# Kernel optimization log

Measured on AMD Instinct MI355X. Metric: run time of the kernel, lower is better.

The kernel has to match this reference:

```python
import jax, jax.numpy as jnp
import numpy as np

DIM = 256
N_QUERY = 4096
N_KEY = 128
SIGMA_PRIOR = 1.0
TEMP = 1.0
LN_EPS = 1e-5


def setup_inputs() -> dict:
    key = jax.random.key(0)
    ks = jax.random.split(key, 16)
    s = 1.0 / np.sqrt(2 * DIM)
    sp = 1.0 / np.sqrt(DIM)
    return {
        "Q": jax.random.normal(ks[0], (N_QUERY, DIM), jnp.float32),
        "K": jax.random.normal(ks[1], (N_QUERY, N_KEY, DIM), jnp.float32),
        "V": jax.random.normal(ks[2], (N_QUERY, N_KEY, DIM), jnp.float32),
        "eps": jax.random.normal(ks[3], (N_QUERY, N_KEY), jnp.float32),
        # mu_posterior_layer: Linear(2*dim,1) split into Q-half and K-half
        "w_mu_q": jax.random.normal(ks[4], (DIM,), jnp.float32) * s,
        "w_mu_k": jax.random.normal(ks[5], (DIM,), jnp.float32) * s,
        "b_mu": jax.random.normal(ks[6], (), jnp.float32) * s,
        # logvar_posterior_layer: Linear(2*dim,1) split
        "w_lv_q": jax.random.normal(ks[7], (DIM,), jnp.float32) * s,
        "w_lv_k": jax.random.normal(ks[8], (DIM,), jnp.float32) * s,
        "b_lv": jax.random.normal(ks[9], (), jnp.float32) * s,
        # mu_prior_layer: Linear(dim,dim) -> ReLU -> Linear(dim,1)
        "W_pr1": jax.random.normal(ks[10], (DIM, DIM), jnp.float32) * sp,
        "b_pr1": jax.random.normal(ks[11], (DIM,), jnp.float32) * sp,
        "w_pr2": jax.random.normal(ks[12], (DIM,), jnp.float32) * sp,
        "b_pr2": jax.random.normal(ks[13], (), jnp.float32) * sp,
        # LayerNorm(dim)
        "gamma": jnp.ones((DIM,), jnp.float32),
        "beta": jnp.zeros((DIM,), jnp.float32),
    }


def reference(Q, K, V, eps, w_mu_q, w_mu_k, b_mu, w_lv_q, w_lv_k, b_lv,
              W_pr1, b_pr1, w_pr2, b_pr2, gamma, beta):
    # ---- prior: small MLP over K -> (n_query, n_key) ----
    h = jax.nn.relu(jnp.einsum('qkd,ed->qke', K, W_pr1) + b_pr1)
    mu_prior = jnp.einsum('qke,e->qk', h, w_pr2) + b_pr2
    mu_prior = mu_prior - SIGMA_PRIOR ** 2 / 2
    sigma_prior = SIGMA_PRIOR
    # ---- posterior: Linear(2*dim,1) on cat([Q_expanded, K]) == split matmuls ----
    q_mu = Q @ w_mu_q                           # (n_query,)
    q_lv = Q @ w_lv_q
    logvar_post = q_lv[:, None] + jnp.einsum('qkd,d->qk', K, w_lv_k) + b_lv
    sigma_post = jnp.exp(0.5 * logvar_post)
    mu_post = q_mu[:, None] + jnp.einsum('qkd,d->qk', K, w_mu_k) + b_mu
    mu_post = mu_post - sigma_post ** 2 / 2
    # ---- KL divergence (mean over all scores) ----
    kl = jnp.mean(jnp.log(sigma_prior / sigma_post)
                  + (sigma_post ** 2 + (mu_post - mu_prior) ** 2) / (2 * sigma_prior ** 2)
                  - 0.5)
    # ---- reparameterized sample (note: original divides by temp twice) ----
    samples = jnp.exp(mu_post + sigma_post * eps) / TEMP
    samples = samples / TEMP
    weights = jax.nn.softmax(samples, axis=-1)   # (n_query, n_key)
    # ---- weighted sum over keys + LayerNorm ----
    context = jnp.einsum('qk,qkd->qd', weights, V)
    mean = jnp.mean(context, axis=-1, keepdims=True)
    var = jnp.mean((context - mean) ** 2, axis=-1, keepdims=True)
    context = (context - mean) * jax.lax.rsqrt(var + LN_EPS) * gamma + beta
    return (context, kl)
```

## Files before the change

kernel.cpp:

```cpp
#include <hip/hip_runtime.h>
#include <hip/hip_bf16.h>
#include <stdint.h>

#define NQ 4096
#define NK 128
#define DIM 256

typedef __attribute__((ext_vector_type(4))) float f32x4;
typedef __attribute__((ext_vector_type(8))) __bf16 bf16x8;
typedef __attribute__((ext_vector_type(8))) unsigned short ushort8;

__device__ __forceinline__ unsigned short f2bf(float x) {
    union { float f; unsigned u; } v; v.f = x;
    unsigned r = v.u + 0x7FFFu + ((v.u >> 16) & 1u);
    return (unsigned short)(r >> 16);
}

__global__ void prep_pack(const float* __restrict__ Wpr1, ushort* __restrict__ Bp) {
    int t = blockIdx.x * 256 + threadIdx.x;
    int lane = t & 63;
    int fid = t >> 6;
    int ctl = fid >> 3;
    int kt  = fid & 7;
    int e = ctl * 16 + (lane & 15);
    int d = kt * 32 + (lane >> 4) * 8;
    const float* src = Wpr1 + (size_t)e * DIM + d;
    ushort* dst = Bp + ((size_t)fid * 64 + lane) * 8;
#pragma unroll
    for (int j = 0; j < 8; j++) dst[j] = f2bf(src[j]);
}

__global__ void prep_qdots(const float* __restrict__ Q,
                           const float* __restrict__ wmq,
                           const float* __restrict__ wlq,
                           float* __restrict__ qmu, float* __restrict__ qlv) {
    int q = blockIdx.x * 4 + (threadIdx.x >> 6);
    int lane = threadIdx.x & 63;
    const float* Qr = Q + (size_t)q * DIM;
    float dm = 0.f, dl = 0.f;
#pragma unroll
    for (int i = lane; i < DIM; i += 64) {
        float x = Qr[i];
        dm += x * wmq[i];
        dl += x * wlq[i];
    }
#pragma unroll
    for (int s = 32; s; s >>= 1) { dm += __shfl_xor(dm, s); dl += __shfl_xor(dl, s); }
    if (lane == 0) { qmu[q] = dm; qlv[q] = dl; }
}

__global__ __launch_bounds__(512, 4) void fused_main(
    const float* __restrict__ K, const float* __restrict__ V,
    const float* __restrict__ eps,
    const float* __restrict__ wmk, const float* __restrict__ bmu_p,
    const float* __restrict__ wlk, const float* __restrict__ blv_p,
    const float* __restrict__ bp1, const float* __restrict__ wp2,
    const float* __restrict__ bp2_p,
    const float* __restrict__ gamma, const float* __restrict__ beta,
    const ushort* __restrict__ Bp,
    const float* __restrict__ qmu, const float* __restrict__ qlv,
    float* __restrict__ klpart, float* __restrict__ out) {

    __shared__ __align__(16) char bigbuf[32768];
    __shared__ __align__(16) float wmk_s[DIM], wlk_s[DIM];
    __shared__ __align__(16) float bp1_s[DIM], wp2_s[DIM];
    __shared__ float smp_s[NK], mu_s[NK], lv_s[NK], wgt_s[NK];
    __shared__ float red_s[8];

    ushort* Blds = (ushort*)bigbuf;
    f32x4*  cpart = (f32x4*)bigbuf;

    const int tid = threadIdx.x;
    const int w = tid >> 6, lane = tid & 63;
    const int q = blockIdx.x;
    const int r15 = lane & 15, g4 = lane >> 4;

    if (tid < DIM) { wmk_s[tid] = wmk[tid]; wlk_s[tid] = wlk[tid]; }
    else { int i = tid - DIM; bp1_s[i] = bp1[i]; wp2_s[i] = wp2[i]; }
    {
        const uint4* src = (const uint4*)Bp;
        uint4* dst = (uint4*)Blds;
#pragma unroll
        for (int i = 0; i < 4; i++) dst[i * 512 + tid] = src[i * 512 + tid];
    }
    __syncthreads();

    const int row = w * 16 + r15;
    const float* Krow = K + ((size_t)q * NK + row) * DIM;
    bf16x8 afrag[8];
    float dm = 0.f, dl = 0.f;
#pragma unroll
    for (int kt = 0; kt < 8; kt++) {
        const int d0 = kt * 32 + g4 * 8;
        float4 x0 = *(const float4*)(Krow + d0);
        float4 x1 = *(const float4*)(Krow + d0 + 4);
        float4 m0 = *(const float4*)(&wmk_s[d0]);
        float4 m1 = *(const float4*)(&wmk_s[d0 + 4]);
        float4 l0 = *(const float4*)(&wlk_s[d0]);
        float4 l1 = *(const float4*)(&wlk_s[d0 + 4]);
        dm += x0.x * m0.x + x0.y * m0.y + x0.z * m0.z + x0.w * m0.w
            + x1.x * m1.x + x1.y * m1.y + x1.z * m1.z + x1.w * m1.w;
        dl += x0.x * l0.x + x0.y * l0.y + x0.z * l0.z + x0.w * l0.w
            + x1.x * l1.x + x1.y * l1.y + x1.z * l1.z + x1.w * l1.w;
        ushort8 u;
        u[0] = f2bf(x0.x); u[1] = f2bf(x0.y); u[2] = f2bf(x0.z); u[3] = f2bf(x0.w);
        u[4] = f2bf(x1.x); u[5] = f2bf(x1.y); u[6] = f2bf(x1.z); u[7] = f2bf(x1.w);
        afrag[kt] = __builtin_bit_cast(bf16x8, u);
    }
    dm += __shfl_xor(dm, 16); dm += __shfl_xor(dm, 32);
    dl += __shfl_xor(dl, 16); dl += __shfl_xor(dl, 32);

    const float b_mu = bmu_p[0], b_lv = blv_p[0], b_pr2 = bp2_p[0];
    {
        const float lv = qlv[q] + dl + b_lv;
        const float sg = expf(0.5f * lv);
        const float mp = qmu[q] + dm + b_mu - 0.5f * sg * sg;
        const float sm = expf(mp + sg * eps[(size_t)q * NK + row]);
        if (g4 == 0) { smp_s[row] = sm; mu_s[row] = mp; lv_s[row] = lv; }
    }
    __syncthreads();

    if (w == 0) {
        float s0 = smp_s[lane], s1 = smp_s[64 + lane];
        float mx = fmaxf(s0, s1);
#pragma unroll
        for (int s = 32; s; s >>= 1) mx = fmaxf(mx, __shfl_xor(mx, s));
        float e0 = expf(s0 - mx), e1 = expf(s1 - mx);
        float sm = e0 + e1;
#pragma unroll
        for (int s = 32; s; s >>= 1) sm += __shfl_xor(sm, s);
        float inv = 1.f / sm;
        wgt_s[lane] = e0 * inv; wgt_s[64 + lane] = e1 * inv;
    }

    f32x4 pm = {0.f, 0.f, 0.f, 0.f};
#pragma unroll
    for (int c = 0; c < 4; c++) {
        if (c) {
            __syncthreads();
            const uint4* src = (const uint4*)Bp;
            uint4* dst = (uint4*)Blds;
#pragma unroll
            for (int i = 0; i < 4; i++)
                dst[i * 512 + tid] = src[(size_t)c * 2048 + i * 512 + tid];
            __syncthreads();
        }
#pragma unroll
        for (int cl = 0; cl < 4; cl++) {
            f32x4 acc = {0.f, 0.f, 0.f, 0.f};
#pragma unroll
            for (int kt = 0; kt < 8; kt++) {
                ushort8 bu = *(const ushort8*)&Blds[((cl * 8 + kt) * 64 + lane) * 8];
                acc = __builtin_amdgcn_mfma_f32_16x16x32_bf16(
                    afrag[kt], __builtin_bit_cast(bf16x8, bu), acc, 0, 0, 0);
            }
            int e = (c * 4 + cl) * 16 + r15;
            float hb = bp1_s[e], wpv = wp2_s[e];
#pragma unroll
            for (int rg = 0; rg < 4; rg++) pm[rg] += fmaxf(acc[rg] + hb, 0.f) * wpv;
        }
    }

#pragma unroll
    for (int s = 1; s < 16; s <<= 1) {
        pm[0] += __shfl_xor(pm[0], s); pm[1] += __shfl_xor(pm[1], s);
        pm[2] += __shfl_xor(pm[2], s); pm[3] += __shfl_xor(pm[3], s);
    }
    {
        float klp = 0.f;
#pragma unroll
        for (int rg = 0; rg < 4; rg++) {
            int rr = w * 16 + g4 * 4 + rg;
            float mup = pm[rg] + b_pr2 - 0.5f;
            float lvr = lv_s[rr];
            float dd = mu_s[rr] - mup;
            klp += -0.5f * lvr + 0.5f * (expf(lvr) + dd * dd) - 0.5f;
        }
        klp += __shfl_xor(klp, 16); klp += __shfl_xor(klp, 32);
        if (lane == 0) red_s[w] = klp;
    }
    __syncthreads();

    f32x4 c4 = {0.f, 0.f, 0.f, 0.f};
    const f32x4* V4 = (const f32x4*)(V + (size_t)q * NK * DIM);
#pragma unroll
    for (int kk = 0; kk < 16; kk++) {
        int k = w * 16 + kk;
        float wk = wgt_s[k];
        f32x4 v = V4[k * 64 + lane];
        c4 += v * wk;
    }
    cpart[w * 64 + lane] = c4;
    __syncthreads();

    if (w == 0) {
        f32x4 t = cpart[lane];
#pragma unroll
        for (int j = 1; j < 8; j++) t += cpart[j * 64 + lane];
        float s1 = t[0] + t[1] + t[2] + t[3];
        float s2 = t[0] * t[0] + t[1] * t[1] + t[2] * t[2] + t[3] * t[3];
#pragma unroll
        for (int s = 32; s; s >>= 1) { s1 += __shfl_xor(s1, s); s2 += __shfl_xor(s2, s); }
        float mean = s1 * (1.f / 256.f);
        float var = s2 * (1.f / 256.f) - mean * mean;
        float rin = rsqrtf(var + 1e-5f);
        f32x4 gv = *(const f32x4*)(gamma + lane * 4);
        f32x4 bv = *(const f32x4*)(beta + lane * 4);
        f32x4 o;
#pragma unroll
        for (int c = 0; c < 4; c++) o[c] = (t[c] - mean) * rin * gv[c] + bv[c];
        *(f32x4*)(out + (size_t)q * DIM + lane * 4) = o;
        if (lane == 0) {
            klpart[q] = red_s[0] + red_s[1] + red_s[2] + red_s[3]
                      + red_s[4] + red_s[5] + red_s[6] + red_s[7];
        }
    }
}

__global__ void finalize(const float* __restrict__ klpart, float* __restrict__ out) {
    __shared__ float red[4];
    int t = threadIdx.x;
    float s = 0.f;
    for (int i = t; i < NQ; i += 256) s += klpart[i];
#pragma unroll
    for (int sh = 32; sh; sh >>= 1) s += __shfl_xor(s, sh);
    if ((t & 63) == 0) red[t >> 6] = s;
    __syncthreads();
    if (t == 0) out[(size_t)NQ * DIM] = (red[0] + red[1] + red[2] + red[3]) * (1.f / ((float)NQ * NK));
}

extern "C" void kernel_launch(void* const* d_in, const int* in_sizes, int n_in,
                              void* d_out, int out_size, void* d_ws, size_t ws_size,
                              hipStream_t stream) {
    const float* Q   = (const float*)d_in[0];
    const float* K   = (const float*)d_in[1];
    const float* V   = (const float*)d_in[2];
    const float* eps = (const float*)d_in[3];
    const float* wmq = (const float*)d_in[4];
    const float* wmk = (const float*)d_in[5];
    const float* bmu = (const float*)d_in[6];
    const float* wlq = (const float*)d_in[7];
    const float* wlk = (const float*)d_in[8];
    const float* blv = (const float*)d_in[9];
    const float* Wp1 = (const float*)d_in[10];
    const float* bp1 = (const float*)d_in[11];
    const float* wp2 = (const float*)d_in[12];
    const float* bp2 = (const float*)d_in[13];
    const float* gam = (const float*)d_in[14];
    const float* bet = (const float*)d_in[15];
    float* out = (float*)d_out;

    char* ws = (char*)d_ws;
    float* qmu    = (float*)(ws + 1024);
    float* qlv    = (float*)(ws + 1024 + 16384);
    float* klpart = (float*)(ws + 1024 + 32768);
    ushort* Bp    = (ushort*)(ws + 65536);

    prep_pack<<<32, 256, 0, stream>>>(Wp1, Bp);
    prep_qdots<<<1024, 256, 0, stream>>>(Q, wmq, wlq, qmu, qlv);
    fused_main<<<NQ, 512, 0, stream>>>(K, V, eps, wmk, bmu, wlk, blv, bp1, wp2, bp2,
                                       gam, bet, Bp, qmu, qlv, klpart, out);
    finalize<<<1, 256, 0, stream>>>(klpart, out);
}
```

Before: 240.9 us.

## Read packed prior weights directly from global memory instead of staging in LDS

Removes the shared-memory staging of the packed bf16 W_pr1 fragments, the small weight vectors and the per-chunk syncthreads, and has each wave load B fragments and bias/weight vectors straight from global (cache-resident) memory. The aim is to remove LDS copy traffic, barriers and LDS footprint (raising occupancy potential). The cost is that every wave now issues its own global loads for the 128KB packed weight, relying on L2/L1 hits and added load latency in the MFMA loop.

```diff
diff --git a/kernel.cpp b/kernel.cpp
--- a/kernel.cpp
+++ b/kernel.cpp
@@ -47,6 +47,10 @@
 #pragma unroll
     for (int s = 32; s; s >>= 1) { dm += __shfl_xor(dm, s); dl += __shfl_xor(dl, s); }
     if (lane == 0) { qmu[q] = dm; qlv[q] = dl; }
+}
+
+__device__ __forceinline__ float dot4(float4 a, float4 b) {
+    return a.x * b.x + a.y * b.y + a.z * b.z + a.w * b.w;
 }
 
 __global__ __launch_bounds__(512, 4) void fused_main(
@@ -61,30 +65,15 @@
     const float* __restrict__ qmu, const float* __restrict__ qlv,
     float* __restrict__ klpart, float* __restrict__ out) {
 
-    __shared__ __align__(16) char bigbuf[32768];
-    __shared__ __align__(16) float wmk_s[DIM], wlk_s[DIM];
-    __shared__ __align__(16) float bp1_s[DIM], wp2_s[DIM];
     __shared__ float smp_s[NK], mu_s[NK], lv_s[NK], wgt_s[NK];
+    __shared__ f32x4 cpart[512];
     __shared__ float red_s[8];
-
-    ushort* Blds = (ushort*)bigbuf;
-    f32x4*  cpart = (f32x4*)bigbuf;
 
     const int tid = threadIdx.x;
     const int w = tid >> 6, lane = tid & 63;
     const int q = blockIdx.x;
     const int r15 = lane & 15, g4 = lane >> 4;
 
-    if (tid < DIM) { wmk_s[tid] = wmk[tid]; wlk_s[tid] = wlk[tid]; }
-    else { int i = tid - DIM; bp1_s[i] = bp1[i]; wp2_s[i] = wp2[i]; }
-    {
-        const uint4* src = (const uint4*)Bp;
-        uint4* dst = (uint4*)Blds;
-#pragma unroll
-        for (int i = 0; i < 4; i++) dst[i * 512 + tid] = src[i * 512 + tid];
-    }
-    __syncthreads();
-
     const int row = w * 16 + r15;
     const float* Krow = K + ((size_t)q * NK + row) * DIM;
     bf16x8 afrag[8];
@@ -94,14 +83,12 @@
         const int d0 = kt * 32 + g4 * 8;
         float4 x0 = *(const float4*)(Krow + d0);
         float4 x1 = *(const float4*)(Krow + d0 + 4);
-        float4 m0 = *(const float4*)(&wmk_s[d0]);
-        float4 m1 = *(const float4*)(&wmk_s[d0 + 4]);
-        float4 l0 = *(const float4*)(&wlk_s[d0]);
-        float4 l1 = *(const float4*)(&wlk_s[d0 + 4]);
-        dm += x0.x * m0.x + x0.y * m0.y + x0.z * m0.z + x0.w * m0.w
-            + x1.x * m1.x + x1.y * m1.y + x1.z * m1.z + x1.w * m1.w;
-        dl += x0.x * l0.x + x0.y * l0.y + x0.z * l0.z + x0.w * l0.w
-            + x1.x * l1.x + x1.y * l1.y + x1.z * l1.z + x1.w * l1.w;
+        float4 m0 = *(const float4*)(wmk + d0);
+        float4 m1 = *(const float4*)(wmk + d0 + 4);
+        float4 l0 = *(const float4*)(wlk + d0);
+        float4 l1 = *(const float4*)(wlk + d0 + 4);
+        dm += dot4(x0, m0) + dot4(x1, m1);
+        dl += dot4(x0, l0) + dot4(x1, l1);
         ushort8 u;
         u[0] = f2bf(x0.x); u[1] = f2bf(x0.y); u[2] = f2bf(x0.z); u[3] = f2bf(x0.w);
         u[4] = f2bf(x1.x); u[5] = f2bf(x1.y); u[6] = f2bf(x1.z); u[7] = f2bf(x1.w);
@@ -134,31 +121,20 @@
     }
 
     f32x4 pm = {0.f, 0.f, 0.f, 0.f};
-#pragma unroll
-    for (int c = 0; c < 4; c++) {
-        if (c) {
-            __syncthreads();
-            const uint4* src = (const uint4*)Bp;
-            uint4* dst = (uint4*)Blds;
-#pragma unroll
-            for (int i = 0; i < 4; i++)
-                dst[i * 512 + tid] = src[(size_t)c * 2048 + i * 512 + tid];
-            __syncthreads();
+    const ushort8* Bg = (const ushort8*)Bp;
+#pragma unroll
+    for (int ctl = 0; ctl < 16; ctl++) {
+        f32x4 acc = {0.f, 0.f, 0.f, 0.f};
+#pragma unroll
+        for (int kt = 0; kt < 8; kt++) {
+            ushort8 bu = Bg[(ctl * 8 + kt) * 64 + lane];
+            acc = __builtin_amdgcn_mfma_f32_16x16x32_bf16(
+                afrag[kt], __builtin_bit_cast(bf16x8, bu), acc, 0, 0, 0);
         }
-#pragma unroll
-        for (int cl = 0; cl < 4; cl++) {
-            f32x4 acc = {0.f, 0.f, 0.f, 0.f};
-#pragma unroll
-            for (int kt = 0; kt < 8; kt++) {
-                ushort8 bu = *(const ushort8*)&Blds[((cl * 8 + kt) * 64 + lane) * 8];
-                acc = __builtin_amdgcn_mfma_f32_16x16x32_bf16(
-                    afrag[kt], __builtin_bit_cast(bf16x8, bu), acc, 0, 0, 0);
-            }
-            int e = (c * 4 + cl) * 16 + r15;
-            float hb = bp1_s[e], wpv = wp2_s[e];
-#pragma unroll
-            for (int rg = 0; rg < 4; rg++) pm[rg] += fmaxf(acc[rg] + hb, 0.f) * wpv;
-        }
+        int e = ctl * 16 + r15;
+        float hb = bp1[e], wpv = wp2[e];
+#pragma unroll
+        for (int rg = 0; rg < 4; rg++) pm[rg] += fmaxf(acc[rg] + hb, 0.f) * wpv;
     }
 
 #pragma unroll
```

Measured after the change: 354.0 us. 47.0% more time.
